# Kernel tuning notes

Hardware: AMD Instinct MI355X
Metric: run time of the kernel (lower is better)

The kernel has to match this reference:

```python
import jax, jax.numpy as jnp
import numpy as np

VOCAB = 401
E = 256   # embed_size
H = 768   # hidden_size
O = 3     # output_size
B = 64
T = 1024


def setup_inputs() -> dict:
    key = jax.random.key(0)
    ks = jax.random.split(key, 8)
    s = lambda fan_in: 1.0 / np.sqrt(fan_in)
    return {
        "tokens": jax.random.randint(ks[0], (B, T), 0, VOCAB),
        "hidden": jnp.zeros((B, H), dtype=jnp.float32),
        "embed": jax.random.normal(ks[1], (VOCAB, E), dtype=jnp.float32),
        "W_ih": jax.random.uniform(ks[2], (3 * H, E), jnp.float32, -s(H), s(H)),
        "W_hh": jax.random.uniform(ks[3], (3 * H, H), jnp.float32, -s(H), s(H)),
        "b_ih": jax.random.uniform(ks[4], (3 * H,), jnp.float32, -s(H), s(H)),
        "b_hh": jax.random.uniform(ks[5], (3 * H,), jnp.float32, -s(H), s(H)),
        "W_out": jax.random.uniform(ks[6], (O, H), jnp.float32, -s(H), s(H)),
        "b_out": jax.random.uniform(ks[7], (O,), jnp.float32, -s(H), s(H)),
    }


def reference(tokens, hidden, embed, W_ih, W_hh, b_ih, b_hh, W_out, b_out):
    # Embedding lookup for all timesteps: [B, T, E]
    x = embed[tokens]
    # Precompute input-to-hidden projections for all steps: [B, T, 3H]
    xi = jnp.einsum("bte,ge->btg", x, W_ih) + b_ih
    # Note: original forward zeroes the passed-in hidden; we honor that.
    h0 = jnp.zeros_like(hidden)

    def step(h, xt):  # xt: [B, 3H]
        gh = h @ W_hh.T + b_hh                      # [B, 3H]
        xr, xz, xn = jnp.split(xt, 3, axis=1)
        hr, hz, hn = jnp.split(gh, 3, axis=1)
        r = jax.nn.sigmoid(xr + hr)
        z = jax.nn.sigmoid(xz + hz)
        n = jnp.tanh(xn + r * hn)
        h_new = (1.0 - z) * n + z * h
        return h_new, None

    h_final, _ = jax.lax.scan(step, h0, jnp.swapaxes(xi, 0, 1))  # scan over T
    logits = h_final @ W_out.T + b_out                            # [B, O]
    logprobs = jax.nn.log_softmax(logits, axis=1)
    return (logprobs, h_final)
```

## Files before the change

kernel.cpp:

```cpp
#include <hip/hip_runtime.h>

#define VOCABN 401
#define EN 256
#define HN 768
#define H3N 2304
#define ON 3
#define BN 64
#define TN 1024

#define NREP 16
#define WGPR 16
#define BPR  4
#define JPW  48
#define NTH  768

typedef _Float16 f16x2 __attribute__((ext_vector_type(2)));
typedef _Float16 f16x8 __attribute__((ext_vector_type(8)));
typedef unsigned long long u64;
union F16x8 { f16x8 v; f16x2 p[4]; };

__device__ __forceinline__ float fdot2(f16x2 a, f16x2 b, float c) {
#if __has_builtin(__builtin_amdgcn_fdot2)
    return __builtin_amdgcn_fdot2(a, b, c, false);
#else
    return c + (float)a[0] * (float)b[0] + (float)a[1] * (float)b[1];
#endif
}

__device__ __forceinline__ float hexsum(float x) {
    int v = __builtin_bit_cast(int, x);
    x += __builtin_bit_cast(float, __builtin_amdgcn_update_dpp(0, v, 0xB1, 0xF, 0xF, true));
    v = __builtin_bit_cast(int, x);
    x += __builtin_bit_cast(float, __builtin_amdgcn_update_dpp(0, v, 0x4E, 0xF, 0xF, true));
    v = __builtin_bit_cast(int, x);
    x += __builtin_bit_cast(float, __builtin_amdgcn_update_dpp(0, v, 0x141, 0xF, 0xF, true));
    v = __builtin_bit_cast(int, x);
    x += __builtin_bit_cast(float, __builtin_amdgcn_update_dpp(0, v, 0x140, 0xF, 0xF, true));
    return x;
}

__global__ __launch_bounds__(256)
void k_build_gtab(const float* __restrict__ embed, const float* __restrict__ wih,
                  const float* __restrict__ bih, float* __restrict__ gtab) {
    const int g  = blockIdx.x * 64 + (threadIdx.x >> 2);
    const int ql = threadIdx.x & 3;
    const int v0 = blockIdx.y * 26;
    const int v1 = min(VOCABN, v0 + 26);
    float4 w[16];
    const float4* s4 = (const float4*)(wih + (size_t)g * EN + ql * 64);
#pragma unroll
    for (int i = 0; i < 16; ++i) w[i] = s4[i];
    const float bias = bih[g];
    for (int v = v0; v < v1; ++v) {
        const float4* e4 = (const float4*)(embed + (size_t)v * EN + ql * 64);
        float acc = 0.f;
#pragma unroll
        for (int i = 0; i < 16; ++i) {
            float4 e = e4[i];
            acc += w[i].x * e.x + w[i].y * e.y + w[i].z * e.z + w[i].w * e.w;
        }
        acc += __shfl_xor(acc, 1, 64);
        acc += __shfl_xor(acc, 2, 64);
        if (ql == 0) gtab[(size_t)v * H3N + g] = acc + bias;
    }
}

__global__ __launch_bounds__(NTH, 1)
void k_rnn(const int* __restrict__ tokens, const float* __restrict__ whh,
           const float* __restrict__ gtab, const float* __restrict__ bhh,
           unsigned* __restrict__ hbuf, float* __restrict__ hout) {
    const int R   = blockIdx.x & (NREP - 1);
    const int wg  = blockIdx.x >> 4;
    const int tid = threadIdx.x;
    const int jl  = tid >> 4;
    const int q   = tid & 15;
    const int j   = wg * JPW + jl;

    __shared__ __align__(16) _Float16 hlds[BPR * 16 * 56];

    F16x8 w[3][6];
#pragma unroll
    for (int g = 0; g < 3; ++g) {
        const float4* s4 = (const float4*)(whh + (size_t)(g * HN + j) * HN + q * 48);
#pragma unroll
        for (int c = 0; c < 6; ++c) {
            float4 a = s4[2 * c], b4 = s4[2 * c + 1];
            F16x8 t;
            t.v[0] = (_Float16)a.x;  t.v[1] = (_Float16)a.y;
            t.v[2] = (_Float16)a.z;  t.v[3] = (_Float16)a.w;
            t.v[4] = (_Float16)b4.x; t.v[5] = (_Float16)b4.y;
            t.v[6] = (_Float16)b4.z; t.v[7] = (_Float16)b4.w;
            w[g][c] = t;
        }
    }

    const float bhr = bhh[j], bhz = bhh[HN + j], bhn = bhh[2 * HN + j];
    u64* hb2 = (u64*)hbuf + (size_t)R * (2 * BPR * 384);
    const int s_   = tid / 24;
    const int off_ = (tid % 24) * 2;
    unsigned short* dep = (unsigned short*)hlds + s_ * 56 + off_;

    float hprev = 0.f;
    float xr = 0.f, xz = 0.f, xn = 0.f, xrn = 0.f, xzn = 0.f, xnn = 0.f;
    if (q < BPR) {
        const int tok = tokens[(size_t)(R * BPR + q) * TN + 0];
        const float* g_ = gtab + (size_t)tok * H3N;
        xr = g_[j]; xz = g_[HN + j]; xn = g_[2 * HN + j];
    }
    u64 v = 0, vn = 0;
    if (tid < 384)
        v = __hip_atomic_load(hb2 + tid, __ATOMIC_RELAXED, __HIP_MEMORY_SCOPE_AGENT);

#pragma unroll 1
    for (int t = 0; t < TN; ++t) {
#pragma unroll
        for (int b = 0; b < BPR; ++b) {
            if (tid < 384) {
                const u64* cur = hb2 + ((t & 1) * BPR + b) * 384 + tid;
                const unsigned want = (unsigned)t;
                while (((((unsigned)(v >> 16)) & 0xffffu) != want) |
                       (((unsigned)(v >> 48)) != want)) {
                    __builtin_amdgcn_s_sleep(1);
                    v = __hip_atomic_load(cur, __ATOMIC_RELAXED, __HIP_MEMORY_SCOPE_AGENT);
                }
                *(unsigned*)(dep + b * 896) =
                    (((unsigned)(v >> 32)) << 16) | ((unsigned)v & 0xffffu);
            }
            __syncthreads();

            if (tid < 384 && !(t == TN - 1 && b == BPR - 1)) {
                const int nb  = (b + 1) & 3;
                const int ntp = (b == 3) ? (t + 1) : t;
                vn = __hip_atomic_load(hb2 + ((ntp & 1) * BPR + nb) * 384 + tid,
                                       __ATOMIC_RELAXED, __HIP_MEMORY_SCOPE_AGENT);
            }
            if (b == 0 && q < BPR && t < TN - 1) {
                const int tok = tokens[(size_t)(R * BPR + q) * TN + (t + 1)];
                const float* g_ = gtab + (size_t)tok * H3N;
                xrn = g_[j]; xzn = g_[HN + j]; xnn = g_[2 * HN + j];
            }

            float ar = 0.f, az = 0.f, an = 0.f;
            const f16x8* hp = (const f16x8*)(hlds + b * 896 + q * 56);
#pragma unroll
            for (int c = 0; c < 6; ++c) {
                F16x8 hh; hh.v = hp[c];
#pragma unroll
                for (int p = 0; p < 4; ++p) {
                    ar = fdot2(w[0][c].p[p], hh.p[p], ar);
                    az = fdot2(w[1][c].p[p], hh.p[p], az);
                    an = fdot2(w[2][c].p[p], hh.p[p], an);
                }
            }
            const float sr = hexsum(ar), sz = hexsum(az), sn = hexsum(an);

            unsigned pk = 0;
            if (q == b) {
                const float r  = 1.f / (1.f + __expf(-(xr + sr + bhr)));
                const float z  = 1.f / (1.f + __expf(-(xz + sz + bhz)));
                const float nx = xn + r * (sn + bhn);
                const float n  = 1.f - 2.f / (__expf(2.f * nx) + 1.f);
                hprev = (1.f - z) * n + z * hprev;
                pk = ((unsigned)(t + 1) << 16)
                   | (unsigned)__builtin_bit_cast(unsigned short, (_Float16)hprev);
            }
            const unsigned pk2 = __shfl_down(pk, 16, 64);
            if (q == b) {
                if (t < TN - 1) {
                    if (!(jl & 1))
                        __hip_atomic_store(
                            hb2 + (((t + 1) & 1) * BPR + b) * 384 + wg * 24 + (jl >> 1),
                            (u64)pk | ((u64)pk2 << 32),
                            __ATOMIC_RELAXED, __HIP_MEMORY_SCOPE_AGENT);
                } else {
                    hout[(size_t)(R * BPR + b) * HN + j] = hprev;
                }
            }
            v = vn;
        }
        xr = xrn; xz = xzn; xn = xnn;
    }
}

__global__ void k_logits(const float* __restrict__ hfin, const float* __restrict__ wout,
                         const float* __restrict__ bout, float* __restrict__ lp) {
    const int b = blockIdx.x;
    const int o = threadIdx.x / 64;
    const int lane = threadIdx.x % 64;
    const float* hrow = hfin + (size_t)b * HN;
    const float* w = wout + (size_t)o * HN;
    float p = 0.f;
    for (int k = lane; k < HN; k += 64) p += hrow[k] * w[k];
    for (int off = 32; off > 0; off >>= 1) p += __shfl_down(p, off, 64);
    __shared__ float lg[ON];
    if (lane == 0) lg[o] = p + bout[o];
    __syncthreads();
    if (threadIdx.x == 0) {
        float m = fmaxf(lg[0], fmaxf(lg[1], lg[2]));
        float s = __expf(lg[0] - m) + __expf(lg[1] - m) + __expf(lg[2] - m);
        float ls = __logf(s);
        lp[b * ON + 0] = lg[0] - m - ls;
        lp[b * ON + 1] = lg[1] - m - ls;
        lp[b * ON + 2] = lg[2] - m - ls;
    }
}

extern "C" void kernel_launch(void* const* d_in, const int* in_sizes, int n_in,
                              void* d_out, int out_size, void* d_ws, size_t ws_size,
                              hipStream_t stream) {
    const int*   tokens = (const int*)d_in[0];
    const float* embed  = (const float*)d_in[2];
    const float* wih    = (const float*)d_in[3];
    const float* whh    = (const float*)d_in[4];
    const float* bih    = (const float*)d_in[5];
    const float* bhh    = (const float*)d_in[6];
    const float* wout   = (const float*)d_in[7];
    const float* bout   = (const float*)d_in[8];

    float* out = (float*)d_out;
    char* ws = (char*)d_ws;
    const size_t GTAB_OFF = 0;
    const size_t HBUF_OFF = 3695616;
    float*    gtab = (float*)(ws + GTAB_OFF);
    unsigned* hbuf = (unsigned*)(ws + HBUF_OFF);

    hipMemsetAsync(ws + HBUF_OFF, 0, 393216, stream);

    hipLaunchKernelGGL(k_build_gtab, dim3(H3N / 64, 16), dim3(256), 0, stream,
                       embed, wih, bih, gtab);
    hipLaunchKernelGGL(k_rnn, dim3(NREP * WGPR), dim3(NTH), 0, stream,
                       tokens, whh, gtab, bhh, hbuf, out + BN * ON);
    hipLaunchKernelGGL(k_logits, dim3(BN), dim3(192), 0, stream,
                       out + BN * ON, wout, bout, out);
}
```

Before: 5.327 ms.

## Compact GRU gate math into dedicated threads via LDS and prefetch two slots ahead

Each workgroup's reduced dot products are written to shared memory. After an extra barrier, the nonlinear GRU update runs on a contiguous block of 48 threads per batch row instead of one divergent lane per 16-lane group across all waves. The hidden-state polling now prefetches two sub-steps ahead, the readiness check is a single 64-bit mask compare, and packing uses a byte-permute. The next token's gate inputs are loaded by the owning thread right after it publishes. The aim is less divergence and shorter spin latency, at the cost of a second __syncthreads per sub-step on the serial recurrence path.

```diff
diff --git a/kernel.cpp b/kernel.cpp
--- a/kernel.cpp
+++ b/kernel.cpp
@@ -77,6 +77,7 @@
     const int j   = wg * JPW + jl;
 
     __shared__ __align__(16) _Float16 hlds[BPR * 16 * 56];
+    __shared__ float s_s[3][BPR][JPW];
 
     F16x8 w[3][6];
 #pragma unroll
@@ -94,91 +95,100 @@
         }
     }
 
-    const float bhr = bhh[j], bhz = bhh[HN + j], bhn = bhh[2 * HN + j];
     u64* hb2 = (u64*)hbuf + (size_t)R * (2 * BPR * 384);
-    const int s_   = tid / 24;
-    const int off_ = (tid % 24) * 2;
-    unsigned short* dep = (unsigned short*)hlds + s_ * 56 + off_;
-
-    float hprev = 0.f;
-    float xr = 0.f, xz = 0.f, xn = 0.f, xrn = 0.f, xzn = 0.f, xnn = 0.f;
-    if (q < BPR) {
-        const int tok = tokens[(size_t)(R * BPR + q) * TN + 0];
+    unsigned short* dep = (unsigned short*)hlds + (tid / 24) * 56 + (tid % 24) * 2;
+
+    const int bown  = tid / 48;
+    const int jlown = tid - bown * 48;
+    const int jown  = wg * JPW + jlown;
+    float hprev = 0.f, xr = 0.f, xz = 0.f, xn = 0.f, bhr = 0.f, bhz = 0.f, bhn = 0.f;
+    if (tid < 192) {
+        bhr = bhh[jown]; bhz = bhh[HN + jown]; bhn = bhh[2 * HN + jown];
+        const int tok = tokens[(size_t)(R * BPR + bown) * TN + 0];
         const float* g_ = gtab + (size_t)tok * H3N;
-        xr = g_[j]; xz = g_[HN + j]; xn = g_[2 * HN + j];
-    }
-    u64 v = 0, vn = 0;
-    if (tid < 384)
-        v = __hip_atomic_load(hb2 + tid, __ATOMIC_RELAXED, __HIP_MEMORY_SCOPE_AGENT);
+        xr = g_[jown]; xz = g_[HN + jown]; xn = g_[2 * HN + jown];
+    }
+
+    u64 vcur = 0, vnxt = 0;
+    if (tid < 384) {
+        vcur = __hip_atomic_load(hb2 + 0 * 384 + tid, __ATOMIC_RELAXED, __HIP_MEMORY_SCOPE_AGENT);
+        vnxt = __hip_atomic_load(hb2 + 1 * 384 + tid, __ATOMIC_RELAXED, __HIP_MEMORY_SCOPE_AGENT);
+    }
 
 #pragma unroll 1
     for (int t = 0; t < TN; ++t) {
+        const u64 want_pair = ((u64)(unsigned)t << 16) | ((u64)(unsigned)t << 48);
 #pragma unroll
         for (int b = 0; b < BPR; ++b) {
             if (tid < 384) {
                 const u64* cur = hb2 + ((t & 1) * BPR + b) * 384 + tid;
-                const unsigned want = (unsigned)t;
-                while (((((unsigned)(v >> 16)) & 0xffffu) != want) |
-                       (((unsigned)(v >> 48)) != want)) {
+                while ((vcur & 0xFFFF0000FFFF0000ull) != want_pair) {
                     __builtin_amdgcn_s_sleep(1);
-                    v = __hip_atomic_load(cur, __ATOMIC_RELAXED, __HIP_MEMORY_SCOPE_AGENT);
+                    vcur = __hip_atomic_load(cur, __ATOMIC_RELAXED, __HIP_MEMORY_SCOPE_AGENT);
                 }
                 *(unsigned*)(dep + b * 896) =
-                    (((unsigned)(v >> 32)) << 16) | ((unsigned)v & 0xffffu);
+                    __builtin_amdgcn_perm((unsigned)(vcur >> 32), (unsigned)vcur, 0x05040100);
             }
             __syncthreads();
 
-            if (tid < 384 && !(t == TN - 1 && b == BPR - 1)) {
-                const int nb  = (b + 1) & 3;
-                const int ntp = (b == 3) ? (t + 1) : t;
-                vn = __hip_atomic_load(hb2 + ((ntp & 1) * BPR + nb) * 384 + tid,
-                                       __ATOMIC_RELAXED, __HIP_MEMORY_SCOPE_AGENT);
-            }
-            if (b == 0 && q < BPR && t < TN - 1) {
-                const int tok = tokens[(size_t)(R * BPR + q) * TN + (t + 1)];
-                const float* g_ = gtab + (size_t)tok * H3N;
-                xrn = g_[j]; xzn = g_[HN + j]; xnn = g_[2 * HN + j];
-            }
-
-            float ar = 0.f, az = 0.f, an = 0.f;
-            const f16x8* hp = (const f16x8*)(hlds + b * 896 + q * 56);
-#pragma unroll
-            for (int c = 0; c < 6; ++c) {
-                F16x8 hh; hh.v = hp[c];
-#pragma unroll
-                for (int p = 0; p < 4; ++p) {
-                    ar = fdot2(w[0][c].p[p], hh.p[p], ar);
-                    az = fdot2(w[1][c].p[p], hh.p[p], az);
-                    an = fdot2(w[2][c].p[p], hh.p[p], an);
-                }
-            }
-            const float sr = hexsum(ar), sz = hexsum(az), sn = hexsum(an);
-
-            unsigned pk = 0;
-            if (q == b) {
+            if (tid < 384) {
+                int b2 = b + 2;
+                const int t2 = t + (b2 >> 2);
+                b2 &= 3;
+                u64 vnew = 0;
+                if (t2 < TN)
+                    vnew = __hip_atomic_load(hb2 + ((t2 & 1) * BPR + b2) * 384 + tid,
+                                             __ATOMIC_RELAXED, __HIP_MEMORY_SCOPE_AGENT);
+                vcur = vnxt;
+                vnxt = vnew;
+            }
+
+            {
+                float ar = 0.f, az = 0.f, an = 0.f;
+                const f16x8* hp = (const f16x8*)(hlds + b * 896 + q * 56);
+#pragma unroll
+                for (int c = 0; c < 6; ++c) {
+                    F16x8 hh; hh.v = hp[c];
+#pragma unroll
+                    for (int p = 0; p < 4; ++p) {
+                        ar = fdot2(w[0][c].p[p], hh.p[p], ar);
+                        az = fdot2(w[1][c].p[p], hh.p[p], az);
+                        an = fdot2(w[2][c].p[p], hh.p[p], an);
+                    }
+                }
+                ar = hexsum(ar); az = hexsum(az); an = hexsum(an);
+                if (q == 0) {
+                    s_s[0][b][jl] = ar; s_s[1][b][jl] = az; s_s[2][b][jl] = an;
+                }
+            }
+            __syncthreads();
+
+            if ((unsigned)(tid - b * 48) < 48u) {
+                const float sr = s_s[0][b][jlown];
+                const float sz = s_s[1][b][jlown];
+                const float sn = s_s[2][b][jlown];
                 const float r  = 1.f / (1.f + __expf(-(xr + sr + bhr)));
                 const float z  = 1.f / (1.f + __expf(-(xz + sz + bhz)));
                 const float nx = xn + r * (sn + bhn);
                 const float n  = 1.f - 2.f / (__expf(2.f * nx) + 1.f);
                 hprev = (1.f - z) * n + z * hprev;
-                pk = ((unsigned)(t + 1) << 16)
-                   | (unsigned)__builtin_bit_cast(unsigned short, (_Float16)hprev);
-            }
-            const unsigned pk2 = __shfl_down(pk, 16, 64);
-            if (q == b) {
+                unsigned pk = ((unsigned)(t + 1) << 16)
+                    | (unsigned)__builtin_bit_cast(unsigned short, (_Float16)hprev);
+                const unsigned pk2 = __shfl_down(pk, 1, 64);
                 if (t < TN - 1) {
-                    if (!(jl & 1))
+                    if (!(jlown & 1))
                         __hip_atomic_store(
-                            hb2 + (((t + 1) & 1) * BPR + b) * 384 + wg * 24 + (jl >> 1),
+                            hb2 + (((t + 1) & 1) * BPR + b) * 384 + wg * 24 + (jlown >> 1),
                             (u64)pk | ((u64)pk2 << 32),
                             __ATOMIC_RELAXED, __HIP_MEMORY_SCOPE_AGENT);
+                    const int tok = tokens[(size_t)(R * BPR + bown) * TN + (t + 1)];
+                    const float* g_ = gtab + (size_t)tok * H3N;
+                    xr = g_[jown]; xz = g_[HN + jown]; xn = g_[2 * HN + jown];
                 } else {
-                    hout[(size_t)(R * BPR + b) * HN + j] = hprev;
-                }
-            }
-            v = vn;
+                    hout[(size_t)(R * BPR + bown) * HN + jown] = hprev;
+                }
+            }
         }
-        xr = xrn; xz = xzn; xn = xnn;
     }
 }
 
```

New measurement: 5.522 ms. 1.04x slower.
